# Performance work log

Hardware: AMD Instinct MI355X
Metric: run time of the kernel (lower is better)

## Reference

```python
import jax, jax.numpy as jnp
import numpy as np

EPS = 1e-8  # torch F.cosine_similarity eps

B, H, K = 64, 2048, 256


def setup_inputs() -> dict:
    key = jax.random.key(0)
    k1, k2, k3, k4 = jax.random.split(key, 4)
    input_state = jax.random.normal(k1, (B, H), dtype=jnp.float32)
    knowledge_base = jax.random.normal(k2, (K, B, H), dtype=jnp.float32)
    W = jax.random.normal(k3, (H, H), dtype=jnp.float32) / np.sqrt(H)
    b = jax.random.normal(k4, (H,), dtype=jnp.float32) * 0.02
    return {"input_state": input_state, "knowledge_base": knowledge_base, "W": W, "b": b}


def reference(input_state, knowledge_base, W, b):
    # linear projection (torch Linear: x @ W.T + b)
    q = input_state @ W.T + b                      # [B, H]
    kproj = jnp.einsum('kbh,oh->kbo', knowledge_base, W) + b  # [K, B, H]
    # cosine similarity over last dim, with torch-style eps clamp on norms
    qn = jnp.maximum(jnp.linalg.norm(q, axis=-1), EPS)        # [B]
    kn = jnp.maximum(jnp.linalg.norm(kproj, axis=-1), EPS)    # [K, B]
    dots = jnp.einsum('bh,kbh->kb', q, kproj)                 # [K, B]
    scores = dots / (qn[None, :] * kn)                        # [K, B]
    # softmax over the K knowledge items
    attn = jax.nn.softmax(scores, axis=0)                     # [K, B]
    # output = input + softmax-weighted sum of (raw) knowledge items
    out = input_state + jnp.einsum('kb,kbh->bh', attn, knowledge_base)
    return out
```

## Files before the change

### kernel.cpp

```cpp
#include <hip/hip_runtime.h>
#include <hip/hip_bf16.h>

typedef unsigned short u16;
typedef unsigned int u32;
typedef unsigned long long u64;
typedef __attribute__((ext_vector_type(8))) short short8;
typedef __attribute__((ext_vector_type(4))) float float4v;

#define B_DIM 64
#define H_DIM 2048
#define K_DIM 256
#define NTHR  256

#define WS_WBF   0ull
#define WS_AQ    (8388608ull)
#define WS_Q     (WS_AQ + 524288ull)
#define WS_KN2   (WS_Q + 524288ull)
#define WS_DOTS  (WS_KN2 + 65536ull)
#define WS_KBF   (WS_DOTS + 65536ull)


__device__ __forceinline__ u16 f2bf(float f) {
    unsigned int u = __float_as_uint(f);
    unsigned int r = (u + 0x7fffu + ((u >> 16) & 1u)) >> 16;
    return (u16)r;
}

__device__ __forceinline__ u64 pack4(float4v v) {
    u64 a0 = f2bf(v.x), a1 = f2bf(v.y), a2 = f2bf(v.z), a3 = f2bf(v.w);
    return a0 | (a1 << 16) | (a2 << 32) | (a3 << 48);
}

__device__ __forceinline__ void llds16(const u16* g, const u16* l) {
    __builtin_amdgcn_global_load_lds(
        (__attribute__((address_space(1))) void*)g,
        (__attribute__((address_space(3))) void*)l, 16, 0, 0);
}

__device__ __forceinline__ void tile_granule(const float* __restrict__ src,
                                             u64* __restrict__ dst, int go) {
    const int p   = go >> 17;
    const int rem = go & 131071;
    const int t   = rem >> 11;
    const int rr  = rem & 2047;
    const int r   = rr >> 3;
    const int gg  = rr & 7;
    const int gs  = (((gg >> 1) ^ ((r >> 1) & 3)) << 3) + ((gg & 1) << 2);
    const float4v v = *(const float4v*)&src[((size_t)(p * 256 + r)) * H_DIM + t * 32 + gs];
    dst[go] = pack4(v);
}

__device__ __forceinline__ void gemm0_tile(const u16* __restrict__ Aq, const u16* __restrict__ Wb,
                                           float* __restrict__ qout, u16* As, u16* Bs,
                                           int nt, int ksplit) {
    const int tid = threadIdx.x;
    const int wave = tid >> 6, lane = tid & 63;
    const int l15 = lane & 15, qd = lane >> 4;
    const int wm = wave >> 1, wn = wave & 1;
    const int n0 = nt * 128;
    const int grow = lane >> 2;
    const int gcol = (((lane & 3) ^ ((lane >> 3) & 3)) * 8);
    const int sw = (l15 >> 1) & 3;
    const u16* wbase = Wb + (size_t)(nt >> 1) * 524288 + (size_t)((nt & 1) * 128) * 32
                          + (size_t)lane * 8;
    float4v acc[4][4] = {};
    const int kb0 = ksplit * 512;
    for (int kk = 0; kk < 16; ++kk) {
        const int k0 = kb0 + kk * 32;
        const int t = ksplit * 16 + kk;
        #pragma unroll
        for (int i = 0; i < 2; ++i) {
            const int r = wave * 32 + i * 16;
            llds16(wbase + (size_t)t * 8192 + (size_t)r * 32, &Bs[r * 32]);
            llds16(Aq + (size_t)(r + grow) * H_DIM + k0 + gcol, &As[r * 32]);
        }
        __syncthreads();
        short8 af[4], bf_[4];
        #pragma unroll
        for (int mi = 0; mi < 4; ++mi)
            af[mi] = *(const short8*)&As[(wm * 64 + mi * 16 + l15) * 32 + ((qd ^ sw) * 8)];
        #pragma unroll
        for (int ni = 0; ni < 4; ++ni)
            bf_[ni] = *(const short8*)&Bs[(wn * 64 + ni * 16 + l15) * 32 + ((qd ^ sw) * 8)];
        #pragma unroll
        for (int mi = 0; mi < 4; ++mi)
            #pragma unroll
            for (int ni = 0; ni < 4; ++ni)
                acc[mi][ni] = __builtin_amdgcn_mfma_f32_16x16x32_bf16(af[mi], bf_[ni], acc[mi][ni], 0, 0, 0);
        __syncthreads();
    }
    const int n0w = n0 + wn * 64;
    if (wm == 0) {
        #pragma unroll
        for (int mi = 0; mi < 4; ++mi)
            #pragma unroll
            for (int reg = 0; reg < 4; ++reg) {
                const int m = mi * 16 + qd * 4 + reg;
                #pragma unroll
                for (int ni = 0; ni < 4; ++ni)
                    atomicAdd(&qout[m * H_DIM + n0w + ni * 16 + l15], acc[mi][ni][reg]);
            }
    }
}

__global__ __launch_bounds__(256) void prep_kernel(
        const float* __restrict__ W, const float* __restrict__ input,
        const float* __restrict__ bias, u16* __restrict__ Wb,
        u16* __restrict__ Aq, float* __restrict__ q,
        float* __restrict__ kn2, float* __restrict__ dots) {
    const int gid = blockIdx.x * NTHR + threadIdx.x;
    tile_granule(W, (u64*)Wb, gid);
    if (gid < 65536) {
        u64 v = 0;
        if (gid < 32768) v = pack4(((const float4v*)input)[gid]);
        ((u64*)Aq)[gid] = v;
    }
    if (gid < 32768)
        ((float4v*)q)[gid] = ((const float4v*)bias)[gid & 511];
    if (gid < 4096) ((float4v*)kn2)[gid] = float4v{0.f, 0.f, 0.f, 0.f};
    else if (gid < 8192) ((float4v*)dots)[gid - 4096] = float4v{0.f, 0.f, 0.f, 0.f};
}

__global__ __launch_bounds__(256, 4) void mid_kernel(
        const float* __restrict__ kb, const u16* __restrict__ Aq,
        const u16* __restrict__ Wb, float* __restrict__ q, u16* __restrict__ Kbf) {
    __shared__ __align__(16) u16 As[128 * 32];
    __shared__ __align__(16) u16 Bs[128 * 32];
    const int bid = blockIdx.x;
    if (bid < 64) {
        gemm0_tile(Aq, Wb, q, As, Bs, bid & 15, bid >> 4);
    } else {
        u64* d8 = (u64*)Kbf;
        for (int go = (bid - 64) * NTHR + threadIdx.x; go < 8388608; go += 960 * NTHR)
            tile_granule(kb, d8, go);
    }
}

#define TILE_BODY(T, bfC, a0C, bfN, a0N)                                        \
  {                                                                             \
    const int t_ = (T);                                                         \
    const u16* As_ = lds + (t_ & 3) * 16384;                                    \
    if (t_ + 3 < 64) stageA(t_ + 3);                                            \
    asm volatile("s_waitcnt lgkmcnt(0)" ::: "memory");                          \
    __builtin_amdgcn_sched_barrier(0);                                          \
    __builtin_amdgcn_s_setprio(1);                                              \
    _Pragma("unroll") for (int mi = 0; mi < 4; ++mi)                            \
      _Pragma("unroll") for (int ni = 0; ni < 4; ++ni)                          \
        acc[mi][ni] = __builtin_amdgcn_mfma_f32_16x16x32_bf16(a0C[mi], bfC[ni], acc[mi][ni], 0, 0, 0); \
    __builtin_amdgcn_s_setprio(0);                                              \
    __builtin_amdgcn_sched_barrier(0);                                          \
    _Pragma("unroll") for (int mi = 0; mi < 4; ++mi)                            \
        a0C[mi] = *(const short8*)&As_[aoff + (4 + mi) * 512];                  \
    if (t_ + 1 < 64) {                                                          \
      const u16* Asn_ = lds + ((t_ + 1) & 3) * 16384;                           \
      const u16* Bsn_ = Asn_ + 8192;                                            \
      _Pragma("unroll") for (int ni = 0; ni < 4; ++ni)                          \
          bfN[ni] = *(const short8*)&Bsn_[boff + ni * 512];                     \
      _Pragma("unroll") for (int mi = 0; mi < 4; ++mi)                          \
          a0N[mi] = *(const short8*)&Asn_[aoff + mi * 512];                     \
    }                                                                           \
    if (t_ + 3 < 64) stageB(t_ + 3);                                            \
    if (t_ + 1 < 64) { asm volatile("s_waitcnt lgkmcnt(8)" ::: "memory"); }     \
    else             { asm volatile("s_waitcnt lgkmcnt(0)" ::: "memory"); }     \
    __builtin_amdgcn_sched_barrier(0);                                          \
    __builtin_amdgcn_s_setprio(1);                                              \
    _Pragma("unroll") for (int mi = 0; mi < 4; ++mi)                            \
      _Pragma("unroll") for (int ni = 0; ni < 4; ++ni)                          \
        acc[4 + mi][ni] = __builtin_amdgcn_mfma_f32_16x16x32_bf16(a0C[mi], bfC[ni], acc[4 + mi][ni], 0, 0, 0); \
    __builtin_amdgcn_s_setprio(0);                                              \
    __builtin_amdgcn_sched_barrier(0);                                          \
    if (t_ <= 60) { asm volatile("s_waitcnt vmcnt(4)" ::: "memory"); }          \
    else          { asm volatile("s_waitcnt vmcnt(0)" ::: "memory"); }          \
    __builtin_amdgcn_s_barrier();                                               \
  }

__global__ __launch_bounds__(512, 2) void gemm_kernel(
        const u16* __restrict__ Kbf, const u16* __restrict__ Wb,
        const float* __restrict__ bias, const float* __restrict__ q,
        float* __restrict__ kn2, float* __restrict__ dots) {
    extern __shared__ __align__(16) u16 lds[];
    const int tid = threadIdx.x;
    const int wave = tid >> 6, lane = tid & 63;
    const int l15 = lane & 15, qd = lane >> 4;
    const int wm = wave >> 2, wn = wave & 3;
    const int nt = blockIdx.x & 7, mt = blockIdx.x >> 3;
    const int m0 = mt * 256, n0 = nt * 256;
    const int sw = (l15 >> 1) & 3;

    const u16* srcA = Kbf + (size_t)mt * 524288 + wave * 512 + lane * 8;
    const u16* srcB = Wb  + (size_t)nt * 524288 + wave * 512 + lane * 8;
    u16* dstBase = lds + wave * 512;

    auto stageA = [&](int t) {
        u16* d = dstBase + (t & 3) * 16384;
        const u16* s = srcA + (size_t)t * 8192;
        llds16(s, d);
        llds16(s + 4096, d + 4096);
    };
    auto stageB = [&](int t) {
        u16* d = dstBase + (t & 3) * 16384 + 8192;
        const u16* s = srcB + (size_t)t * 8192;
        llds16(s, d);
        llds16(s + 4096, d + 4096);
    };

    const int aoff = (wm * 128 + l15) * 32 + ((qd ^ sw) * 8);
    const int boff = (wn * 64 + l15) * 32 + ((qd ^ sw) * 8);

    float4v acc[8][4] = {};
    short8 bf0[4], a00[4], bf1[4], a01[4];

    stageA(0); stageB(0); stageA(1); stageB(1); stageA(2); stageB(2);
    asm volatile("s_waitcnt vmcnt(4)" ::: "memory");
    __builtin_amdgcn_sched_barrier(0);
    __builtin_amdgcn_s_barrier();
    {
        const u16* As0 = lds;
        const u16* Bs0 = lds + 8192;
        #pragma unroll
        for (int ni = 0; ni < 4; ++ni) bf0[ni] = *(const short8*)&Bs0[boff + ni * 512];
        #pragma unroll
        for (int mi = 0; mi < 4; ++mi) a00[mi] = *(const short8*)&As0[aoff + mi * 512];
    }

    for (int t = 0; t < 64; t += 2) {
        TILE_BODY(t,     bf0, a00, bf1, a01);
        TILE_BODY(t + 1, bf1, a01, bf0, a00);
    }

    const int n0w = n0 + wn * 64;
    float* red = (float*)lds;
    float bv[4];
    #pragma unroll
    for (int ni = 0; ni < 4; ++ni) bv[ni] = bias[n0w + ni * 16 + l15];
    #pragma unroll
    for (int mi = 0; mi < 8; ++mi)
        #pragma unroll
        for (int reg = 0; reg < 4; ++reg) {
            const int mloc = mi * 16 + qd * 4 + reg;
            const float* qrow = q + (mloc & 63) * H_DIM;
            float s2 = 0.f, sd = 0.f;
            #pragma unroll
            for (int ni = 0; ni < 4; ++ni) {
                const float y = acc[mi][ni][reg] + bv[ni];
                const float qv = qrow[n0w + ni * 16 + l15];
                s2 += y * y; sd += y * qv;
            }
            #pragma unroll
            for (int off = 1; off < 16; off <<= 1) {
                s2 += __shfl_xor(s2, off);
                sd += __shfl_xor(sd, off);
            }
            if (l15 == 0) {
                const int row = wm * 128 + mloc;
                red[wn * 256 + row] = s2;
                red[1024 + wn * 256 + row] = sd;
            }
        }
    __syncthreads();
    if (tid < 256) {
        const float k2 = red[tid] + red[256 + tid] + red[512 + tid] + red[768 + tid];
        const float dd = red[1024 + tid] + red[1280 + tid] + red[1536 + tid] + red[1792 + tid];
        atomicAdd(&kn2[m0 + tid], k2);
        atomicAdd(&dots[m0 + tid], dd);
    }
}

__global__ __launch_bounds__(1024) void final_kernel(
        const float* __restrict__ input, const float* __restrict__ kb,
        const float* __restrict__ q, const float* __restrict__ kn2,
        const float* __restrict__ dots, float* __restrict__ out) {
    __shared__ float sm[K_DIM];
    __shared__ float buf[24];
    __shared__ float2 part[1024];
    const int b = blockIdx.x >> 2, hc = blockIdx.x & 3, tid = threadIdx.x;
    const int wave = tid >> 6, lane = tid & 63;
    float s = 0.f;
    #pragma unroll
    for (int i = 0; i < 2; ++i) {
        float v = q[b * H_DIM + i * 1024 + tid];
        s += v * v;
    }
    #pragma unroll
    for (int o = 32; o >= 1; o >>= 1) s += __shfl_xor(s, o);
    if (lane == 0) buf[wave] = s;
    __syncthreads();
    float qs = 0.f;
    #pragma unroll
    for (int i = 0; i < 16; ++i) qs += buf[i];
    const float qn = fmaxf(sqrtf(qs), 1e-8f);
    __syncthreads();
    float sc = 0.f;
    if (tid < K_DIM) {
        const float kn = fmaxf(sqrtf(kn2[tid * B_DIM + b]), 1e-8f);
        sc = dots[tid * B_DIM + b] / (qn * kn);
        float mx = sc;
        #pragma unroll
        for (int o = 32; o >= 1; o >>= 1) mx = fmaxf(mx, __shfl_xor(mx, o));
        if (lane == 0) buf[16 + wave] = mx;
    }
    __syncthreads();
    const float mx = fmaxf(fmaxf(buf[16], buf[17]), fmaxf(buf[18], buf[19]));
    __syncthreads();
    if (tid < K_DIM) {
        const float e = expf(sc - mx);
        float se = e;
        #pragma unroll
        for (int o = 32; o >= 1; o >>= 1) se += __shfl_xor(se, o);
        if (lane == 0) buf[20 + wave] = se;
        sm[tid] = e;
    }
    __syncthreads();
    const float sei = 1.f / (buf[20] + buf[21] + buf[22] + buf[23]);
    __syncthreads();
    const int col = tid & 255, quarter = tid >> 8;
    const int h2 = hc * 256 + col;
    const float2* basep = (const float2*)kb
        + ((size_t)(quarter * 64 * B_DIM + b)) * (H_DIM / 2) + h2;
    const float* smq = sm + quarter * 64;
    float s0 = 0.f, s1 = 0.f;
    #pragma unroll 8
    for (int i = 0; i < 64; ++i) {
        const float2 p = basep[(size_t)i * (B_DIM * H_DIM / 2)];
        const float a = smq[i];
        s0 += a * p.x;
        s1 += a * p.y;
    }
    part[tid] = float2{s0, s1};
    __syncthreads();
    if (tid < 256) {
        float2 p0 = part[tid], p1 = part[256 + tid], p2 = part[512 + tid], p3 = part[768 + tid];
        const int h = h2 * 2;
        float2 iv = *(const float2*)&input[(size_t)b * H_DIM + h];
        float2 r;
        r.x = iv.x + (p0.x + p1.x + p2.x + p3.x) * sei;
        r.y = iv.y + (p0.y + p1.y + p2.y + p3.y) * sei;
        *(float2*)&out[(size_t)b * H_DIM + h] = r;
    }
}

extern "C" void kernel_launch(void* const* d_in, const int* in_sizes, int n_in,
                              void* d_out, int out_size, void* d_ws, size_t ws_size,
                              hipStream_t stream) {
    const float* input = (const float*)d_in[0];
    const float* kb    = (const float*)d_in[1];
    const float* W     = (const float*)d_in[2];
    const float* bias  = (const float*)d_in[3];
    float* out = (float*)d_out;
    char* ws = (char*)d_ws;

    u16*   Wb   = (u16*)(ws + WS_WBF);
    u16*   Aq   = (u16*)(ws + WS_AQ);
    float* q    = (float*)(ws + WS_Q);
    float* kn2  = (float*)(ws + WS_KN2);
    float* dots = (float*)(ws + WS_DOTS);
    u16*   Kbf  = (u16*)(ws + WS_KBF);

    static int lds_set = 0;
    if (!lds_set) {
        hipFuncSetAttribute((const void*)gemm_kernel,
                            hipFuncAttributeMaxDynamicSharedMemorySize, 131072);
        lds_set = 1;
    }

    prep_kernel<<<4096, NTHR, 0, stream>>>(W, input, bias, Wb, Aq, q, kn2, dots);
    mid_kernel<<<1024, NTHR, 0, stream>>>(kb, Aq, Wb, q, Kbf);
    gemm_kernel<<<512, 512, 131072, stream>>>(Kbf, Wb, bias, q, kn2, dots);
    final_kernel<<<256, 1024, 0, stream>>>(input, kb, q, kn2, dots, out);
}
```

Before: 362.1 us.

## Load W operand directly into registers, stage only A through LDS

The main GEMM now reads the B (weight) fragments straight from global memory into registers one tile ahead, rather than staging them through LDS. Only the A (knowledge) tiles keep the 4-deep LDS ring, which halves dynamic shared memory to 64 KB and cuts LDS traffic. The wait counts and prologue are reworked to fit the new pipeline. The cost is exposed global-load latency on B, since B is prefetched only one tile ahead, and each wave now re-fetches B from global memory and cache instead of sharing it through LDS.

```diff
diff --git a/kernel.cpp b/kernel.cpp
--- a/kernel.cpp
+++ b/kernel.cpp
@@ -136,41 +136,41 @@
     }
 }
 
-#define TILE_BODY(T, bfC, a0C, bfN, a0N)                                        \
+#define TILE_BODY(T, bfC, bfN, aC, aN)                                          \
   {                                                                             \
     const int t_ = (T);                                                         \
-    const u16* As_ = lds + (t_ & 3) * 16384;                                    \
-    if (t_ + 3 < 64) stageA(t_ + 3);                                            \
+    const int tb = (t_ + 1 < 64) ? t_ + 1 : 63;                                 \
+    const int ta = (t_ + 3 < 64) ? t_ + 3 : 63;                                 \
+    loadB(tb, bfN);                                                             \
+    __builtin_amdgcn_sched_barrier(0);                                          \
+    stageA(ta);                                                                 \
     asm volatile("s_waitcnt lgkmcnt(0)" ::: "memory");                          \
     __builtin_amdgcn_sched_barrier(0);                                          \
     __builtin_amdgcn_s_setprio(1);                                              \
     _Pragma("unroll") for (int mi = 0; mi < 4; ++mi)                            \
       _Pragma("unroll") for (int ni = 0; ni < 4; ++ni)                          \
-        acc[mi][ni] = __builtin_amdgcn_mfma_f32_16x16x32_bf16(a0C[mi], bfC[ni], acc[mi][ni], 0, 0, 0); \
+        acc[mi][ni] = __builtin_amdgcn_mfma_f32_16x16x32_bf16(aC[mi], bfC[ni], acc[mi][ni], 0, 0, 0); \
     __builtin_amdgcn_s_setprio(0);                                              \
     __builtin_amdgcn_sched_barrier(0);                                          \
-    _Pragma("unroll") for (int mi = 0; mi < 4; ++mi)                            \
-        a0C[mi] = *(const short8*)&As_[aoff + (4 + mi) * 512];                  \
-    if (t_ + 1 < 64) {                                                          \
-      const u16* Asn_ = lds + ((t_ + 1) & 3) * 16384;                           \
-      const u16* Bsn_ = Asn_ + 8192;                                            \
-      _Pragma("unroll") for (int ni = 0; ni < 4; ++ni)                          \
-          bfN[ni] = *(const short8*)&Bsn_[boff + ni * 512];                     \
+    { const u16* As_ = lds + (t_ & 3) * 8192;                                   \
       _Pragma("unroll") for (int mi = 0; mi < 4; ++mi)                          \
-          a0N[mi] = *(const short8*)&Asn_[aoff + mi * 512];                     \
+        aC[mi] = *(const short8*)&As_[aoff + (4 + mi) * 512];                   \
+      if (t_ + 1 < 64) {                                                        \
+        const u16* Asn_ = lds + ((t_ + 1) & 3) * 8192;                          \
+        _Pragma("unroll") for (int mi = 0; mi < 4; ++mi)                        \
+          aN[mi] = *(const short8*)&Asn_[aoff + mi * 512];                      \
+      }                                                                         \
     }                                                                           \
-    if (t_ + 3 < 64) stageB(t_ + 3);                                            \
-    if (t_ + 1 < 64) { asm volatile("s_waitcnt lgkmcnt(8)" ::: "memory"); }     \
-    else             { asm volatile("s_waitcnt lgkmcnt(0)" ::: "memory"); }     \
+    if (t_ < 63) { asm volatile("s_waitcnt lgkmcnt(4)" ::: "memory"); }         \
+    else         { asm volatile("s_waitcnt lgkmcnt(0)" ::: "memory"); }         \
     __builtin_amdgcn_sched_barrier(0);                                          \
     __builtin_amdgcn_s_setprio(1);                                              \
     _Pragma("unroll") for (int mi = 0; mi < 4; ++mi)                            \
       _Pragma("unroll") for (int ni = 0; ni < 4; ++ni)                          \
-        acc[4 + mi][ni] = __builtin_amdgcn_mfma_f32_16x16x32_bf16(a0C[mi], bfC[ni], acc[4 + mi][ni], 0, 0, 0); \
+        acc[4 + mi][ni] = __builtin_amdgcn_mfma_f32_16x16x32_bf16(aC[mi], bfC[ni], acc[4 + mi][ni], 0, 0, 0); \
     __builtin_amdgcn_s_setprio(0);                                              \
     __builtin_amdgcn_sched_barrier(0);                                          \
-    if (t_ <= 60) { asm volatile("s_waitcnt vmcnt(4)" ::: "memory"); }          \
-    else          { asm volatile("s_waitcnt vmcnt(0)" ::: "memory"); }          \
+    asm volatile("s_waitcnt vmcnt(2)" ::: "memory");                            \
     __builtin_amdgcn_s_barrier();                                               \
   }
 
@@ -188,45 +188,46 @@
     const int sw = (l15 >> 1) & 3;
 
     const u16* srcA = Kbf + (size_t)mt * 524288 + wave * 512 + lane * 8;
-    const u16* srcB = Wb  + (size_t)nt * 524288 + wave * 512 + lane * 8;
     u16* dstBase = lds + wave * 512;
 
     auto stageA = [&](int t) {
-        u16* d = dstBase + (t & 3) * 16384;
+        u16* d = dstBase + (t & 3) * 8192;
         const u16* s = srcA + (size_t)t * 8192;
         llds16(s, d);
         llds16(s + 4096, d + 4096);
     };
-    auto stageB = [&](int t) {
-        u16* d = dstBase + (t & 3) * 16384 + 8192;
-        const u16* s = srcB + (size_t)t * 8192;
-        llds16(s, d);
-        llds16(s + 4096, d + 4096);
+
+    const int rB = wn * 64 + l15;
+    const u16* srcB = Wb + (size_t)nt * 524288 + (size_t)rB * 32 + ((qd ^ sw) * 8);
+    auto loadB = [&](int t, short8* bf) {
+        const u16* bp = srcB + (size_t)t * 8192;
+        bf[0] = *(const short8*)(bp);
+        bf[1] = *(const short8*)(bp + 512);
+        bf[2] = *(const short8*)(bp + 1024);
+        bf[3] = *(const short8*)(bp + 1536);
     };
 
     const int aoff = (wm * 128 + l15) * 32 + ((qd ^ sw) * 8);
-    const int boff = (wn * 64 + l15) * 32 + ((qd ^ sw) * 8);
 
     float4v acc[8][4] = {};
-    short8 bf0[4], a00[4], bf1[4], a01[4];
-
-    stageA(0); stageB(0); stageA(1); stageB(1); stageA(2); stageB(2);
-    asm volatile("s_waitcnt vmcnt(4)" ::: "memory");
+    short8 bf0[4], bf1[4], a0[4], a1v[4];
+
+    loadB(0, bf0);
     __builtin_amdgcn_sched_barrier(0);
+    stageA(0); stageA(1);
+    asm volatile("s_waitcnt vmcnt(0)" ::: "memory");
+    __builtin_amdgcn_sched_barrier(0);
+    stageA(2);
     __builtin_amdgcn_s_barrier();
-    {
-        const u16* As0 = lds;
-        const u16* Bs0 = lds + 8192;
-        #pragma unroll
-        for (int ni = 0; ni < 4; ++ni) bf0[ni] = *(const short8*)&Bs0[boff + ni * 512];
-        #pragma unroll
-        for (int mi = 0; mi < 4; ++mi) a00[mi] = *(const short8*)&As0[aoff + mi * 512];
-    }
+    #pragma unroll
+    for (int mi = 0; mi < 4; ++mi) a0[mi] = *(const short8*)&lds[aoff + mi * 512];
 
     for (int t = 0; t < 64; t += 2) {
-        TILE_BODY(t,     bf0, a00, bf1, a01);
-        TILE_BODY(t + 1, bf1, a01, bf0, a00);
-    }
+        TILE_BODY(t,     bf0, bf1, a0,  a1v);
+        TILE_BODY(t + 1, bf1, bf0, a1v, a0);
+    }
+    asm volatile("s_waitcnt vmcnt(0)" ::: "memory");
+    __builtin_amdgcn_s_barrier();
 
     const int n0w = n0 + wn * 64;
     float* red = (float*)lds;
@@ -359,12 +360,12 @@
     static int lds_set = 0;
     if (!lds_set) {
         hipFuncSetAttribute((const void*)gemm_kernel,
-                            hipFuncAttributeMaxDynamicSharedMemorySize, 131072);
+                            hipFuncAttributeMaxDynamicSharedMemorySize, 65536);
         lds_set = 1;
     }
 
     prep_kernel<<<4096, NTHR, 0, stream>>>(W, input, bias, Wb, Aq, q, kn2, dots);
     mid_kernel<<<1024, NTHR, 0, stream>>>(kb, Aq, Wb, q, Kbf);
-    gemm_kernel<<<512, 512, 131072, stream>>>(Kbf, Wb, bias, q, kn2, dots);
+    gemm_kernel<<<512, 512, 65536, stream>>>(Kbf, Wb, bias, q, kn2, dots);
     final_kernel<<<256, 1024, 0, stream>>>(input, kb, q, kn2, dots, out);
 }
```

After: 379.6 us. +4.8%, slower.

## Read bf16 tiled knowledge base in final kernel and reinterleave GEMM LDS loads

Applied to the files above, without the earlier changes.

The final weighted-sum kernel now reads the knowledge base from the already-converted, tiled and swizzled bf16 copy in the workspace instead of the fp32 input. This halves the bytes streamed in that pass. The cost is bf16 precision in the output accumulation and a more complex address computation. Separately, the GEMM tile body splits the first MFMA group so the A-fragment LDS reloads and the B staging are issued between MFMA halves, and it drops the priority boost on the first group.

```diff
diff --git a/kernel.cpp b/kernel.cpp
--- a/kernel.cpp
+++ b/kernel.cpp
@@ -143,14 +143,18 @@
     if (t_ + 3 < 64) stageA(t_ + 3);                                            \
     asm volatile("s_waitcnt lgkmcnt(0)" ::: "memory");                          \
     __builtin_amdgcn_sched_barrier(0);                                          \
-    __builtin_amdgcn_s_setprio(1);                                              \
-    _Pragma("unroll") for (int mi = 0; mi < 4; ++mi)                            \
+    _Pragma("unroll") for (int mi = 0; mi < 2; ++mi)                            \
       _Pragma("unroll") for (int ni = 0; ni < 4; ++ni)                          \
         acc[mi][ni] = __builtin_amdgcn_mfma_f32_16x16x32_bf16(a0C[mi], bfC[ni], acc[mi][ni], 0, 0, 0); \
-    __builtin_amdgcn_s_setprio(0);                                              \
+    a0C[0] = *(const short8*)&As_[aoff + 4 * 512];                              \
+    a0C[1] = *(const short8*)&As_[aoff + 5 * 512];                              \
+    _Pragma("unroll") for (int mi = 2; mi < 4; ++mi)                            \
+      _Pragma("unroll") for (int ni = 0; ni < 4; ++ni)                          \
+        acc[mi][ni] = __builtin_amdgcn_mfma_f32_16x16x32_bf16(a0C[mi], bfC[ni], acc[mi][ni], 0, 0, 0); \
+    a0C[2] = *(const short8*)&As_[aoff + 6 * 512];                              \
+    a0C[3] = *(const short8*)&As_[aoff + 7 * 512];                              \
+    if (t_ + 3 < 64) stageB(t_ + 3);                                            \
     __builtin_amdgcn_sched_barrier(0);                                          \
-    _Pragma("unroll") for (int mi = 0; mi < 4; ++mi)                            \
-        a0C[mi] = *(const short8*)&As_[aoff + (4 + mi) * 512];                  \
     if (t_ + 1 < 64) {                                                          \
       const u16* Asn_ = lds + ((t_ + 1) & 3) * 16384;                           \
       const u16* Bsn_ = Asn_ + 8192;                                            \
@@ -158,10 +162,10 @@
           bfN[ni] = *(const short8*)&Bsn_[boff + ni * 512];                     \
       _Pragma("unroll") for (int mi = 0; mi < 4; ++mi)                          \
           a0N[mi] = *(const short8*)&Asn_[aoff + mi * 512];                     \
+      asm volatile("s_waitcnt lgkmcnt(8)" ::: "memory");                        \
+    } else {                                                                    \
+      asm volatile("s_waitcnt lgkmcnt(0)" ::: "memory");                        \
     }                                                                           \
-    if (t_ + 3 < 64) stageB(t_ + 3);                                            \
-    if (t_ + 1 < 64) { asm volatile("s_waitcnt lgkmcnt(8)" ::: "memory"); }     \
-    else             { asm volatile("s_waitcnt lgkmcnt(0)" ::: "memory"); }     \
     __builtin_amdgcn_sched_barrier(0);                                          \
     __builtin_amdgcn_s_setprio(1);                                              \
     _Pragma("unroll") for (int mi = 0; mi < 4; ++mi)                            \
@@ -267,7 +271,7 @@
 }
 
 __global__ __launch_bounds__(1024) void final_kernel(
-        const float* __restrict__ input, const float* __restrict__ kb,
+        const float* __restrict__ input, const u16* __restrict__ Kbf,
         const float* __restrict__ q, const float* __restrict__ kn2,
         const float* __restrict__ dots, float* __restrict__ out) {
     __shared__ float sm[K_DIM];
@@ -315,27 +319,32 @@
     __syncthreads();
     const int col = tid & 255, quarter = tid >> 8;
     const int h2 = hc * 256 + col;
-    const float2* basep = (const float2*)kb
-        + ((size_t)(quarter * 64 * B_DIM + b)) * (H_DIM / 2) + h2;
+    const int h = h2 * 2;
+    const int t = h >> 5;
+    const int f = h & 31;
+    const int gsrc = f >> 2;
+    const int sxor = (b >> 1) & 3;
+    const int gg = ((gsrc >> 1) ^ sxor) * 2 + (gsrc & 1);
+    const u32* kp = (const u32*)Kbf + (size_t)quarter * 4194304
+                    + t * 4096 + b * 16 + gg * 2 + ((f >> 1) & 1);
     const float* smq = sm + quarter * 64;
     float s0 = 0.f, s1 = 0.f;
-    #pragma unroll 8
+    #pragma unroll 4
     for (int i = 0; i < 64; ++i) {
-        const float2 p = basep[(size_t)i * (B_DIM * H_DIM / 2)];
+        const u32 p = kp[(size_t)(i >> 2) * 262144 + (i & 3) * 1024];
         const float a = smq[i];
-        s0 += a * p.x;
-        s1 += a * p.y;
+        s0 += a * __uint_as_float(p << 16);
+        s1 += a * __uint_as_float(p & 0xffff0000u);
     }
     part[tid] = float2{s0, s1};
     __syncthreads();
     if (tid < 256) {
         float2 p0 = part[tid], p1 = part[256 + tid], p2 = part[512 + tid], p3 = part[768 + tid];
-        const int h = h2 * 2;
-        float2 iv = *(const float2*)&input[(size_t)b * H_DIM + h];
+        float2 iv = *(const float2*)&input[(size_t)b * H_DIM + h2 * 2];
         float2 r;
         r.x = iv.x + (p0.x + p1.x + p2.x + p3.x) * sei;
         r.y = iv.y + (p0.y + p1.y + p2.y + p3.y) * sei;
-        *(float2*)&out[(size_t)b * H_DIM + h] = r;
+        *(float2*)&out[(size_t)b * H_DIM + h2 * 2] = r;
     }
 }
 
@@ -366,5 +375,5 @@
     prep_kernel<<<4096, NTHR, 0, stream>>>(W, input, bias, Wb, Aq, q, kn2, dots);
     mid_kernel<<<1024, NTHR, 0, stream>>>(kb, Aq, Wb, q, Kbf);
     gemm_kernel<<<512, 512, 131072, stream>>>(Kbf, Wb, bias, q, kn2, dots);
-    final_kernel<<<256, 1024, 0, stream>>>(input, kb, q, kn2, dots, out);
-}
+    final_kernel<<<256, 1024, 0, stream>>>(input, Kbf, q, kn2, dots, out);
+}
```

Result: no change. 365.8 us (+1.0%).
